# Kernel optimization log

Measured on AMD Instinct MI355X. Metric: run time of the kernel, lower is better.

The kernel has to match this reference:

```python
import jax, jax.numpy as jnp
import numpy as np

N, E, G = 50000, 800000, 2000          # nodes, edges, graphs
F_NODE, F_EDGE, H = 64, 16, 128
SLOPE = 0.01                            # leaky_relu slope used throughout AttentiveFP
NUM_ATOM_LAYERS = 2                     # num_layers=3 -> 1 GATEConv + 2 GATConv
NUM_TIMESTEPS = 3


def _leaky(v):
    return jnp.where(v >= 0, v, SLOPE * v)


def _seg_softmax(logits, seg, n):
    # PyG softmax over edges grouped by target segment
    m = jax.ops.segment_max(logits, seg, num_segments=n)
    e = jnp.exp(logits - m[seg])
    s = jax.ops.segment_sum(e, seg, num_segments=n)
    return e / (s[seg] + 1e-16)


def _gru(xi, h, Wih, Whh, bih, bhh):
    # torch.nn.GRUCell, gate order (r, z, n)
    gi = xi @ Wih.T + bih
    gh = h @ Whh.T + bhh
    ir, iz, inn = jnp.split(gi, 3, axis=-1)
    hr, hz, hn = jnp.split(gh, 3, axis=-1)
    r = jax.nn.sigmoid(ir + hr)
    z = jax.nn.sigmoid(iz + hz)
    ng = jnp.tanh(inn + r * hn)
    return (1.0 - z) * ng + z * h


def setup_inputs() -> dict:
    key = jax.random.key(0)
    ks = iter(jax.random.split(key, 64))
    def rn(shape, s=0.1):
        return jax.random.normal(next(ks), shape, jnp.float32) * s
    inp = {}
    inp["x"] = jax.random.normal(next(ks), (N, F_NODE), jnp.float32)
    inp["edge_index"] = jax.random.randint(next(ks), (2, E), 0, N)
    inp["edge_attr"] = jax.random.normal(next(ks), (E, F_EDGE), jnp.float32)
    inp["batch"] = jnp.sort(jax.random.randint(next(ks), (N,), 0, G))
    inp["lin1_W"] = rn((H, F_NODE)); inp["lin1_b"] = rn((H,))
    inp["gate_att_l"] = rn((H,)); inp["gate_att_r"] = rn((H,))
    inp["gate_lin1_W"] = rn((H, H + F_EDGE)); inp["gate_lin2_W"] = rn((H, H)); inp["gate_bias"] = rn((H,))
    inp["gru0_Wih"] = rn((3 * H, H)); inp["gru0_Whh"] = rn((3 * H, H))
    inp["gru0_bih"] = rn((3 * H,)); inp["gru0_bhh"] = rn((3 * H,))
    L = NUM_ATOM_LAYERS
    inp["atom_lin_W"] = rn((L, H, H)); inp["atom_att_src"] = rn((L, H))
    inp["atom_att_dst"] = rn((L, H)); inp["atom_bias"] = rn((L, H))
    inp["atom_gru_Wih"] = rn((L, 3 * H, H)); inp["atom_gru_Whh"] = rn((L, 3 * H, H))
    inp["atom_gru_bih"] = rn((L, 3 * H)); inp["atom_gru_bhh"] = rn((L, 3 * H))
    inp["mol_lin_W"] = rn((H, H)); inp["mol_att_src"] = rn((H,))
    inp["mol_att_dst"] = rn((H,)); inp["mol_bias"] = rn((H,))
    inp["mol_gru_Wih"] = rn((3 * H, H)); inp["mol_gru_Whh"] = rn((3 * H, H))
    inp["mol_gru_bih"] = rn((3 * H,)); inp["mol_gru_bhh"] = rn((3 * H,))
    inp["lin2_W"] = rn((H, H)); inp["lin2_b"] = rn((H,))
    inp["fin_W"] = rn((1, H)); inp["fin_b"] = rn((1,))
    return inp


def _forward(x, edge_attr, lin1_W, lin1_b, gate_att_l, gate_att_r, gate_lin1_W,
             gate_lin2_W, gate_bias, gru0_Wih, gru0_Whh, gru0_bih, gru0_bhh,
             atom_lin_W, atom_att_src, atom_att_dst, atom_bias,
             atom_gru_Wih, atom_gru_Whh, atom_gru_bih, atom_gru_bhh,
             mol_lin_W, mol_att_src, mol_att_dst, mol_bias,
             mol_gru_Wih, mol_gru_Whh, mol_gru_bih, mol_gru_bhh,
             lin2_W, lin2_b, fin_W, fin_b, edge_index, batch):
    src, dst = edge_index[0], edge_index[1]  # PyG: row=source j, col=target i
    # --- input projection ---
    x = _leaky(x @ lin1_W.T + lin1_b)                                     # [N,H]
    # --- GATEConv (edge-featured attention, add aggregation) ---
    hj = _leaky(jnp.concatenate([x[src], edge_attr], axis=-1) @ gate_lin1_W.T)  # [E,H]
    alpha = _leaky(hj @ gate_att_l + (x @ gate_att_r)[dst])               # [E]
    a = _seg_softmax(alpha, dst, N)
    h = jax.ops.segment_sum((x @ gate_lin2_W.T)[src] * a[:, None], dst, num_segments=N) + gate_bias
    h = jax.nn.elu(h)  # dropout is identity in eval mode
    x = jnp.maximum(_gru(h, x, gru0_Wih, gru0_Whh, gru0_bih, gru0_bhh), 0.0)
    # --- atom-level GATConv layers (single head, no self loops) ---
    for l in range(NUM_ATOM_LAYERS):
        xs = x @ atom_lin_W[l].T                                          # [N,H]
        a = _leaky((xs @ atom_att_src[l])[src] + (xs @ atom_att_dst[l])[dst])
        a = _seg_softmax(a, dst, N)
        h = jax.ops.segment_sum(xs[src] * a[:, None], dst, num_segments=N) + atom_bias[l]
        h = jax.nn.elu(h)
        x = jnp.maximum(_gru(h, x, atom_gru_Wih[l], atom_gru_Whh[l],
                             atom_gru_bih[l], atom_gru_bhh[l]), 0.0)
    # --- molecule-level readout: bipartite GATConv node->graph + GRU ---
    out = jnp.maximum(jax.ops.segment_sum(x, batch, num_segments=G), 0.0)  # [G,H]
    xs = x @ mol_lin_W.T                                                   # fixed sources
    a_src = xs @ mol_att_src                                               # [N]
    for _ in range(NUM_TIMESTEPS):
        od = out @ mol_lin_W.T                                             # [G,H]
        a = _leaky(a_src + (od @ mol_att_dst)[batch])
        a = _seg_softmax(a, batch, G)
        h = jax.ops.segment_sum(xs * a[:, None], batch, num_segments=G) + mol_bias
        h = jax.nn.elu(h)
        out = jnp.maximum(_gru(h, out, mol_gru_Wih, mol_gru_Whh, mol_gru_bih, mol_gru_bhh), 0.0)
    out = out @ lin2_W.T + lin2_b                                          # AttentiveFP.lin2
    return jax.nn.sigmoid(out @ fin_W.T + fin_b).squeeze(-1)               # [G]


def reference(x, edge_index, edge_attr, batch, lin1_W, lin1_b, gate_att_l, gate_att_r,
              gate_lin1_W, gate_lin2_W, gate_bias, gru0_Wih, gru0_Whh, gru0_bih, gru0_bhh,
              atom_lin_W, atom_att_src, atom_att_dst, atom_bias,
              atom_gru_Wih, atom_gru_Whh, atom_gru_bih, atom_gru_bhh,
              mol_lin_W, mol_att_src, mol_att_dst, mol_bias,
              mol_gru_Wih, mol_gru_Whh, mol_gru_bih, mol_gru_bhh,
              lin2_W, lin2_b, fin_W, fin_b):
    return _forward(x, edge_attr, lin1_W, lin1_b, gate_att_l, gate_att_r, gate_lin1_W,
                    gate_lin2_W, gate_bias, gru0_Wih, gru0_Whh, gru0_bih, gru0_bhh,
                    atom_lin_W, atom_att_src, atom_att_dst, atom_bias,
                    atom_gru_Wih, atom_gru_Whh, atom_gru_bih, atom_gru_bhh,
                    mol_lin_W, mol_att_src, mol_att_dst, mol_bias,
                    mol_gru_Wih, mol_gru_Whh, mol_gru_bih, mol_gru_bhh,
                    lin2_W, lin2_b, fin_W, fin_b, edge_index, batch)
```

## Files before the change

### kernel.cpp

```cpp
#include <hip/hip_runtime.h>
#include <math.h>

#define NN 50000
#define EE 800000
#define GG 2000
#define HH 128
#define FN 64
#define FE 16

typedef short bf16x8 __attribute__((ext_vector_type(8)));
typedef float f32x4  __attribute__((ext_vector_type(4)));

__device__ __forceinline__ float leakyf(float v){ return v>=0.f ? v : 0.01f*v; }
__device__ __forceinline__ float eluf(float v){ return v>0.f ? v : expm1f(v); }
__device__ __forceinline__ float sigmf(float v){ return 1.f/(1.f+__expf(-v)); }
__device__ __forceinline__ float tanh_fast(float x){
  float ax = fabsf(x);
  float e = __expf(-2.f*ax);
  float t = (1.f - e)/(1.f + e);
  return x>=0.f ? t : -t;
}
__device__ __forceinline__ int rdl(int v, int l){ return __builtin_amdgcn_readlane(v, l); }
__device__ __forceinline__ float rdlf(float v, int l){
  return __int_as_float(__builtin_amdgcn_readlane(__float_as_int(v), l));
}
__device__ __forceinline__ float wsum(float v){
#pragma unroll
  for(int m=32;m>=1;m>>=1) v += __shfl_xor(v,m,64);
  return v;
}
__device__ __forceinline__ float wsum16(float v){
#pragma unroll
  for(int m=8;m>=1;m>>=1) v += __shfl_xor(v,m,64);
  return v;
}
__device__ __forceinline__ float wmax64(float v){
#pragma unroll
  for(int m=32;m>=1;m>>=1) v = fmaxf(v,__shfl_xor(v,m,64));
  return v;
}

__device__ __forceinline__ f32x4 mfma16(bf16x8 a, bf16x8 b, f32x4 c){
  return __builtin_amdgcn_mfma_f32_16x16x32_bf16(a, b, c, 0, 0, 0);
}

__device__ __forceinline__ void splitbf8(const float* p, bf16x8 &hi, bf16x8 &lo){
  float4 u = *(const float4*)p;
  float4 v = *(const float4*)(p+4);
  float f[8] = {u.x,u.y,u.z,u.w,v.x,v.y,v.z,v.w};
#pragma unroll
  for(int i=0;i<8;i++){
    unsigned b = __float_as_uint(f[i]);
    unsigned ht = b & 0xFFFF0000u;
    hi[i] = (short)(b >> 16);
    float r = f[i] - __uint_as_float(ht);
    lo[i] = (short)(__float_as_uint(r) >> 16);
  }
}

#define CV_LIN1   0
#define CV_G1X    8192
#define CV_G2     24576
#define CV_ALIN   40960
#define CV_MOL    73728
#define CV_G0IH   90112
#define CV_G0HH   139264
#define CV_AIH    188416
#define CV_AHH    286720
#define CV_MIH    385024
#define CV_MHH    434176
#define CV_TOT    483328

__global__ void k_convw2(const float* __restrict__ lin1W, const float* __restrict__ glin1W,
                         const float* __restrict__ glin2W, const float* __restrict__ aLinW,
                         const float* __restrict__ aGWih, const float* __restrict__ aGWhh,
                         const float* __restrict__ mLinW, const float* __restrict__ mGWih,
                         const float* __restrict__ mGWhh, const float* __restrict__ g0Wih,
                         const float* __restrict__ g0Whh,
                         short* __restrict__ hi, short* __restrict__ lo){
  int i = blockIdx.x*256 + threadIdx.x;
  if(i >= CV_TOT) return;
  float v;
  if(i < CV_G1X){            v = lin1W[i];
  } else if(i < CV_G2){      int idx = i - CV_G1X; v = glin1W[(size_t)(idx>>7)*144 + (idx&127)];
  } else if(i < CV_ALIN){    v = glin2W[i - CV_G2];
  } else if(i < CV_MOL){     v = aLinW[i - CV_ALIN];
  } else if(i < CV_G0IH){    v = mLinW[i - CV_MOL];
  } else if(i < CV_G0HH){    v = g0Wih[i - CV_G0IH];
  } else if(i < CV_AIH){     v = g0Whh[i - CV_G0HH];
  } else if(i < CV_AHH){     v = aGWih[i - CV_AIH];
  } else if(i < CV_MIH){     v = aGWhh[i - CV_AHH];
  } else if(i < CV_MHH){     v = mGWih[i - CV_MIH];
  } else {                   v = mGWhh[i - CV_MHH];
  }
  unsigned b = __float_as_uint(v);
  unsigned ht = b & 0xFFFF0000u;
  hi[i] = (short)(b >> 16);
  float r = v - __uint_as_float(ht);
  lo[i] = (short)(__float_as_uint(r) >> 16);
}

__global__ void k_count_all(const int* __restrict__ esrc, const int* __restrict__ edst,
                            const int* __restrict__ batch,
                            int* __restrict__ degd, int* __restrict__ degs,
                            int* __restrict__ gcnt){
  int i = blockIdx.x*256 + threadIdx.x;
  if(i < EE){
    atomicAdd(&degd[edst[i]], 1);
    atomicAdd(&degs[esrc[i]], 1);
  }
  if(i < NN) atomicAdd(&gcnt[batch[i]], 1);
}

__global__ void k_scan3(const int* __restrict__ degd, const int* __restrict__ degs,
                        const int* __restrict__ gcnt,
                        int* __restrict__ eoff, int* __restrict__ soff, int* __restrict__ goff){
  __shared__ int part[1024];
  const int* cnt; int* off; int n;
  if(blockIdx.x == 0){ cnt = degd; off = eoff; n = NN; }
  else if(blockIdx.x == 1){ cnt = degs; off = soff; n = NN; }
  else { cnt = gcnt; off = goff; n = GG; }
  int t = threadIdx.x;
  int C = (n + 1023) >> 10;
  int lo = t*C, hic = min(lo + C, n);
  int s = 0;
  for(int i=lo;i<hic;i++) s += cnt[i];
  part[t] = s;
  __syncthreads();
  for(int o=1;o<1024;o<<=1){
    int v = (t>=o) ? part[t-o] : 0;
    __syncthreads();
    part[t] += v;
    __syncthreads();
  }
  int base = part[t] - s;
  int run = base;
  for(int i=lo;i<hic;i++){ run += cnt[i]; off[i+1] = run; }
  if(t==0) off[0] = 0;
}

__global__ void k_scatter2(const int* __restrict__ esrc, const int* __restrict__ edst,
                           const int* __restrict__ eoff, const int* __restrict__ soff,
                           int* __restrict__ curd, int* __restrict__ curs,
                           int* __restrict__ esrcS, int* __restrict__ eperm,
                           int* __restrict__ eord){
  int e = blockIdx.x*256 + threadIdx.x;
  if(e < EE){
    int d = edst[e];
    int pos = eoff[d] + atomicAdd(&curd[d], 1);
    esrcS[pos] = esrc[e];
    eperm[e] = pos;
    int s = esrc[e];
    int pos2 = soff[s] + atomicAdd(&curs[s], 1);
    eord[pos2] = e;
  }
}

template<int ACT, int K, int NDOT>
__global__ __launch_bounds__(256) void k_proj_mfma(const float* __restrict__ A,
                                                   const short* __restrict__ Whi,
                                                   const short* __restrict__ Wlo,
                                                   const float* __restrict__ bias,
                                                   float* __restrict__ C, int M,
                                                   const float* __restrict__ u,
                                                   const float* __restrict__ v,
                                                   float* __restrict__ douta,
                                                   float* __restrict__ doutb){
  const int wave = threadIdx.x >> 6, lane = threadIdx.x & 63;
  const int m0 = blockIdx.x*64 + wave*16;
  const int lr = lane & 15, kg = lane >> 4;
  f32x4 acc[8];
#pragma unroll
  for(int t=0;t<8;t++) acc[t] = (f32x4){0.f,0.f,0.f,0.f};

  int arow = m0 + lr;
  int ar = arow < M ? arow : (M-1);

#pragma unroll
  for(int ks=0;ks<K;ks+=32){
    const int kb = ks + kg*8;
    bf16x8 ahi, alo;
    splitbf8(&A[(size_t)ar*K + kb], ahi, alo);
#pragma unroll
    for(int t=0;t<8;t++){
      const bf16x8 bh = *(const bf16x8*)&Whi[(size_t)(t*16+lr)*K + kb];
      const bf16x8 bl = *(const bf16x8*)&Wlo[(size_t)(t*16+lr)*K + kb];
      acc[t] = mfma16(ahi, bh, acc[t]);
      acc[t] = mfma16(ahi, bl, acc[t]);
      acc[t] = mfma16(alo, bh, acc[t]);
    }
  }

  float p1[4] = {0.f,0.f,0.f,0.f};
  float p2[4] = {0.f,0.f,0.f,0.f};
#pragma unroll
  for(int t=0;t<8;t++){
    int c = t*16 + lr;
    float ut = (NDOT>=1) ? u[c] : 0.f;
    float vt = (NDOT>=2) ? v[c] : 0.f;
#pragma unroll
    for(int r=0;r<4;r++){
      int m = m0 + kg*4 + r;
      float val = acc[t][r];
      if(ACT==1) val = leakyf(val + bias[c]);
      if(m < M) C[(size_t)m*HH + c] = val;
      if(NDOT>=1) p1[r] += val*ut;
      if(NDOT>=2) p2[r] += val*vt;
    }
  }
  if(NDOT>=1){
#pragma unroll
    for(int r=0;r<4;r++){
      float s1 = wsum16(p1[r]);
      int m = m0 + kg*4 + r;
      if(lr==0 && m < M) douta[m] = s1;
      if(NDOT>=2){
        float s2 = wsum16(p2[r]);
        if(lr==0 && m < M) doutb[m] = s2;
      }
    }
  }
}

__global__ __launch_bounds__(256) void k_gru_mfma(const float* __restrict__ MSG,
                                                  const float* __restrict__ X,
                                                  const short* __restrict__ WIhi,
                                                  const short* __restrict__ WIlo,
                                                  const short* __restrict__ WHhi,
                                                  const short* __restrict__ WHlo,
                                                  const float* __restrict__ bih,
                                                  const float* __restrict__ bhh,
                                                  float* __restrict__ XOUT, int M){
  __shared__ short LW[12*16*128];
  const int tid = threadIdx.x;
  const int wave = tid >> 6, lane = tid & 63;
  const int m0 = blockIdx.x*64 + wave*16;
  const int lr = lane & 15, kg = lane >> 4;
  int arow = m0 + lr;
  int ar = arow < M ? arow : (M-1);

  bf16x8 mh[4], ml[4], xh[4], xl[4];
#pragma unroll
  for(int ks=0;ks<4;ks++){
    splitbf8(&MSG[(size_t)ar*HH + ks*32 + kg*8], mh[ks], ml[ks]);
    splitbf8(&X  [(size_t)ar*HH + ks*32 + kg*8], xh[ks], xl[ks]);
  }

  const int srow = tid >> 4;
  const int scb  = tid & 15;
  const int sdst = srow*128 + ((scb ^ (srow & 7))*8);
  const size_t sgoff = (size_t)srow*HH + scb*8;

#pragma unroll 1
  for(int t=0;t<8;t++){
#pragma unroll
    for(int r=0;r<12;r++){
      const short* mat = (r<3) ? WIhi : (r<6) ? WHhi : (r<9) ? WIlo : WHlo;
      const int g = (r % 3);
      const short* src = mat + (size_t)(g*128 + t*16)*HH + sgoff;
      *(bf16x8*)&LW[r*2048 + sdst] = *(const bf16x8*)src;
    }
    __syncthreads();

    f32x4 aIr = (f32x4){0.f,0.f,0.f,0.f}, aIz = aIr, aIn = aIr;
    f32x4 aHr = aIr, aHz = aIr, aHn = aIr;
#pragma unroll
    for(int ks=0;ks<4;ks++){
      const int cb = ks*4 + kg;
      const int rb = lr*128 + ((cb ^ (lr & 7))*8);
      bf16x8 bIrh = *(const bf16x8*)&LW[ 0*2048 + rb];
      bf16x8 bIzh = *(const bf16x8*)&LW[ 1*2048 + rb];
      bf16x8 bInh = *(const bf16x8*)&LW[ 2*2048 + rb];
      bf16x8 bHrh = *(const bf16x8*)&LW[ 3*2048 + rb];
      bf16x8 bHzh = *(const bf16x8*)&LW[ 4*2048 + rb];
      bf16x8 bHnh = *(const bf16x8*)&LW[ 5*2048 + rb];
      bf16x8 bIrl = *(const bf16x8*)&LW[ 6*2048 + rb];
      bf16x8 bIzl = *(const bf16x8*)&LW[ 7*2048 + rb];
      bf16x8 bInl = *(const bf16x8*)&LW[ 8*2048 + rb];
      bf16x8 bHrl = *(const bf16x8*)&LW[ 9*2048 + rb];
      bf16x8 bHzl = *(const bf16x8*)&LW[10*2048 + rb];
      bf16x8 bHnl = *(const bf16x8*)&LW[11*2048 + rb];
      aIr = mfma16(mh[ks], bIrh, aIr); aIr = mfma16(mh[ks], bIrl, aIr); aIr = mfma16(ml[ks], bIrh, aIr);
      aIz = mfma16(mh[ks], bIzh, aIz); aIz = mfma16(mh[ks], bIzl, aIz); aIz = mfma16(ml[ks], bIzh, aIz);
      aIn = mfma16(mh[ks], bInh, aIn); aIn = mfma16(mh[ks], bInl, aIn); aIn = mfma16(ml[ks], bInh, aIn);
      aHr = mfma16(xh[ks], bHrh, aHr); aHr = mfma16(xh[ks], bHrl, aHr); aHr = mfma16(xl[ks], bHrh, aHr);
      aHz = mfma16(xh[ks], bHzh, aHz); aHz = mfma16(xh[ks], bHzl, aHz); aHz = mfma16(xl[ks], bHzh, aHz);
      aHn = mfma16(xh[ks], bHnh, aHn); aHn = mfma16(xh[ks], bHnl, aHn); aHn = mfma16(xl[ks], bHnh, aHn);
    }

    const int c = t*16 + lr;
    const float bir = bih[c], biz = bih[c+HH], bin = bih[c+2*HH];
    const float bhr = bhh[c], bhz = bhh[c+HH], bhn = bhh[c+2*HH];
#pragma unroll
    for(int r=0;r<4;r++){
      int mm = m0 + kg*4 + r;
      if(mm < M){
        float ir = aIr[r]+bir, iz = aIz[r]+biz, in_ = aIn[r]+bin;
        float hr = aHr[r]+bhr, hz = aHz[r]+bhz, hn = aHn[r]+bhn;
        float rr = sigmf(ir + hr);
        float z  = sigmf(iz + hz);
        float ng = tanh_fast(in_ + rr*hn);
        float hp = X[(size_t)mm*HH + c];
        XOUT[(size_t)mm*HH + c] = fmaxf((1.f - z)*ng + z*hp, 0.f);
      }
    }
    __syncthreads();
  }
}

__global__ __launch_bounds__(256) void k_gate_alpha3(const float* __restrict__ XP,
                                                     const float* __restrict__ EA,
                                                     const int* __restrict__ esrc,
                                                     const int* __restrict__ edst,
                                                     const float* __restrict__ W1,
                                                     const float* __restrict__ attl,
                                                     const float* __restrict__ RD,
                                                     const int* __restrict__ eperm,
                                                     const int* __restrict__ eord,
                                                     float* __restrict__ ALPHA){
  __shared__ float W1E[128*16];
  __shared__ float ATTL[128];
  const int tid = threadIdx.x;
#pragma unroll
  for(int q=0;q<8;q++){
    int idx = tid*8 + q;
    int c = idx >> 4, f = idx & 15;
    W1E[idx] = W1[(size_t)c*144 + 128 + f];
  }
  if(tid < 128) ATTL[tid] = attl[tid];
  __syncthreads();

  const int p = blockIdx.x*256 + tid;
  const int eo = eord[p];
  const int s  = esrc[eo];
  const int d  = edst[eo];
  const int pd = eperm[eo];

  float ea[16];
  {
    const float4* g = (const float4*)&EA[(size_t)eo*FE];
    float4 v0=g[0], v1=g[1], v2=g[2], v3=g[3];
    ea[0]=v0.x;ea[1]=v0.y;ea[2]=v0.z;ea[3]=v0.w;
    ea[4]=v1.x;ea[5]=v1.y;ea[6]=v1.z;ea[7]=v1.w;
    ea[8]=v2.x;ea[9]=v2.y;ea[10]=v2.z;ea[11]=v2.w;
    ea[12]=v3.x;ea[13]=v3.y;ea[14]=v3.z;ea[15]=v3.w;
  }

  float acc = 0.f;
#pragma unroll 4
  for(int c0=0;c0<HH;c0+=4){
    float4 xp = *(const float4*)&XP[(size_t)s*HH + c0];
    float xpv[4] = {xp.x, xp.y, xp.z, xp.w};
#pragma unroll
    for(int cc=0;cc<4;cc++){
      const float* wr = &W1E[(c0+cc)*16];
      float eaw = 0.f;
#pragma unroll
      for(int f=0;f<16;f++) eaw += ea[f]*wr[f];
      acc += leakyf(xpv[cc] + eaw) * ATTL[c0+cc];
    }
  }
  ALPHA[pd] = leakyf(acc + RD[d]);
}

template<int MODE>
__global__ void k_softmaxw(const int* __restrict__ off, const int* __restrict__ items,
                           const float* __restrict__ AIN, const float* __restrict__ A1,
                           const float* __restrict__ A2, float* __restrict__ WOUT, int nseg){
  int w = (blockIdx.x*blockDim.x + threadIdx.x) >> 6;
  int lane = threadIdx.x & 63;
  if(w >= nseg) return;
  int s0 = off[w], s1 = off[w+1];
  int n = s1 - s0;
  float a2 = (MODE==0) ? 0.f : A2[w];

  if(n <= 64){
    float a = -INFINITY;
    int i = s0 + lane;
    if(lane < n){
      if(MODE==0) a = AIN[i];
      else if(MODE==1) a = leakyf(A1[items[i]] + a2);
      else a = leakyf(A1[i] + a2);
    }
    float m = wmax64(a);
    float e = (lane < n) ? __expf(a - m) : 0.f;
    float s = wsum(e);
    if(lane < n) WOUT[i] = e/(s + 1e-16f);
    return;
  }

  float m = -INFINITY;
  for(int i=s0+lane;i<s1;i+=64){
    float a;
    if(MODE==0) a = AIN[i];
    else if(MODE==1) a = leakyf(A1[items[i]] + a2);
    else a = leakyf(A1[i] + a2);
    m = fmaxf(m, a);
  }
  m = wmax64(m);

  float s = 0.f;
  for(int i=s0+lane;i<s1;i+=64){
    float a;
    if(MODE==0) a = AIN[i];
    else if(MODE==1) a = leakyf(A1[items[i]] + a2);
    else a = leakyf(A1[i] + a2);
    s += __expf(a - m);
  }
  s = wsum(s);
  float inv = 1.f/(s + 1e-16f);

  for(int i=s0+lane;i<s1;i+=64){
    float a;
    if(MODE==0) a = AIN[i];
    else if(MODE==1) a = leakyf(A1[items[i]] + a2);
    else a = leakyf(A1[i] + a2);
    WOUT[i] = __expf(a - m)*inv;
  }
}

__global__ void k_gather(const int* __restrict__ off, const int* __restrict__ items,
                         const float* __restrict__ W, const float* __restrict__ XSrc,
                         const float* __restrict__ bias, float* __restrict__ OUT, int nseg){
  int w = (blockIdx.x*blockDim.x + threadIdx.x) >> 6;
  int lane = threadIdx.x & 63;
  if(w >= nseg) return;
  int s0 = off[w], s1 = off[w+1];
  float hx = 0.f, hy = 0.f;

  for(int c0=s0;c0<s1;c0+=64){
    int n = min(64, s1-c0);
    int it = 0; float wg = 0.f;
    if(lane < n){
      int i = c0 + lane;
      it = items ? items[i] : i;
      wg = W[i];
    }
#pragma unroll 16
    for(int j=0;j<n;j++){
      int itj = rdl(it, j);
      float wj = rdlf(wg, j);
      float2 xv = *(const float2*)&XSrc[(size_t)itj*HH + 2*lane];
      hx += wj*xv.x;
      hy += wj*xv.y;
    }
  }
  float2 bv = *(const float2*)&bias[2*lane];
  float2 o;
  o.x = eluf(hx + bv.x);
  o.y = eluf(hy + bv.y);
  *(float2*)&OUT[(size_t)w*HH + 2*lane] = o;
}

__global__ void k_dot2(const float* __restrict__ X, const float* __restrict__ u,
                       float* __restrict__ a, int M){
  int w = (blockIdx.x*blockDim.x + threadIdx.x) >> 6;
  int lane = threadIdx.x & 63;
  if(w >= M) return;
  float2 x = *(const float2*)&X[(size_t)w*HH + 2*lane];
  float2 uu = *(const float2*)&u[2*lane];
  float p = x.x*uu.x + x.y*uu.y;
  p = wsum(p);
  if(lane==0) a[w] = p;
}

__global__ void k_ginit(const int* __restrict__ goff, const float* __restrict__ X,
                        float* __restrict__ OUT){
  int g = (blockIdx.x*blockDim.x + threadIdx.x) >> 6;
  int lane = threadIdx.x & 63;
  if(g >= GG) return;
  int s0 = goff[g], s1 = goff[g+1];
  float hx=0.f, hy=0.f;
  for(int n=s0;n<s1;n++){
    float2 xv = *(const float2*)&X[(size_t)n*HH + 2*lane];
    hx += xv.x; hy += xv.y;
  }
  float2 o;
  o.x = fmaxf(hx, 0.f);
  o.y = fmaxf(hy, 0.f);
  *(float2*)&OUT[(size_t)g*HH + 2*lane] = o;
}

__global__ void k_weff(const float* __restrict__ lin2W, const float* __restrict__ lin2b,
                       const float* __restrict__ finW, const float* __restrict__ finb,
                       const float* __restrict__ mLinW, const float* __restrict__ mAttD,
                       float* __restrict__ weff){
  int c = threadIdx.x;
  float s = 0.f, q = 0.f;
  for(int j=0;j<HH;j++){
    s += finW[j]*lin2W[(size_t)j*HH + c];
    q += mAttD[j]*mLinW[(size_t)j*HH + c];
  }
  weff[c] = s;
  weff[256 + c] = q;
  if(c==0){
    float bb = finb[0];
    for(int j=0;j<HH;j++) bb += lin2b[j]*finW[j];
    weff[HH] = bb;
  }
}

__global__ void k_final(const float* __restrict__ OUT, const float* __restrict__ weff,
                        float* __restrict__ y){
  int g = (blockIdx.x*blockDim.x + threadIdx.x) >> 6;
  int lane = threadIdx.x & 63;
  if(g >= GG) return;
  float2 ov = *(const float2*)&OUT[(size_t)g*HH + 2*lane];
  float2 wv = *(const float2*)&weff[2*lane];
  float p = ov.x*wv.x + ov.y*wv.y;
  p = wsum(p);
  if(lane==0) y[g] = sigmf(p + weff[HH]);
}

extern "C" void kernel_launch(void* const* d_in, const int* in_sizes, int n_in,
                              void* d_out, int out_size, void* d_ws, size_t ws_size,
                              hipStream_t stream){
  const float* in_x   = (const float*)d_in[0];
  const int*   eidx   = (const int*)d_in[1];
  const float* ea     = (const float*)d_in[2];
  const int*   batch  = (const int*)d_in[3];
  const float* lin1W  = (const float*)d_in[4];
  const float* lin1b  = (const float*)d_in[5];
  const float* gattl  = (const float*)d_in[6];
  const float* gattr  = (const float*)d_in[7];
  const float* glin1W = (const float*)d_in[8];
  const float* glin2W = (const float*)d_in[9];
  const float* gbias  = (const float*)d_in[10];
  const float* g0Wih  = (const float*)d_in[11];
  const float* g0Whh  = (const float*)d_in[12];
  const float* g0bih  = (const float*)d_in[13];
  const float* g0bhh  = (const float*)d_in[14];
  const float* aLinW  = (const float*)d_in[15];
  const float* aAttS  = (const float*)d_in[16];
  const float* aAttD  = (const float*)d_in[17];
  const float* aBias  = (const float*)d_in[18];
  const float* aGWih  = (const float*)d_in[19];
  const float* aGWhh  = (const float*)d_in[20];
  const float* aGbih  = (const float*)d_in[21];
  const float* aGbhh  = (const float*)d_in[22];
  const float* mLinW  = (const float*)d_in[23];
  const float* mAttS  = (const float*)d_in[24];
  const float* mAttD  = (const float*)d_in[25];
  const float* mBias  = (const float*)d_in[26];
  const float* mGWih  = (const float*)d_in[27];
  const float* mGWhh  = (const float*)d_in[28];
  const float* mGbih  = (const float*)d_in[29];
  const float* mGbhh  = (const float*)d_in[30];
  const float* lin2W  = (const float*)d_in[31];
  const float* lin2b  = (const float*)d_in[32];
  const float* finW   = (const float*)d_in[33];
  const float* finb   = (const float*)d_in[34];

  const int* esrc0 = eidx;
  const int* edst0 = eidx + EE;

  char* w = (char*)d_ws;
  size_t o = 0;
  auto alloc = [&](size_t bytes)->void*{
    void* p = w + o;
    o = (o + bytes + 255) & ~(size_t)255;
    return p;
  };
  float* X    = (float*)alloc((size_t)NN*HH*4);
  float* XB   = (float*)alloc((size_t)NN*HH*4);
  float* XS   = (float*)alloc((size_t)NN*HH*4);
  float* MSG  = (float*)alloc((size_t)NN*HH*4);
  float* XP   = (float*)alloc((size_t)NN*HH*4);
  float* ALPHA= (float*)alloc((size_t)EE*4);
  float* S1   = (float*)alloc((size_t)NN*4);
  float* S2   = (float*)alloc((size_t)NN*4);
  float* ADSTG= (float*)alloc((size_t)GG*4);
  float* OUTg = (float*)alloc((size_t)GG*HH*4);
  float* OUTb = (float*)alloc((size_t)GG*HH*4);
  float* HG   = (float*)alloc((size_t)GG*HH*4);
  float* WEFF = (float*)alloc(512*4);
  short* cWhi = (short*)alloc((size_t)CV_TOT*2);
  short* cWlo = (short*)alloc((size_t)CV_TOT*2);
  int* zeroreg= (int*)alloc((size_t)(4*NN + 2048)*4);
  int* degd = zeroreg;
  int* degs = zeroreg + NN;
  int* curd = zeroreg + 2*NN;
  int* curs = zeroreg + 3*NN;
  int* gcnt = zeroreg + 4*NN;
  int* eoff = (int*)alloc((size_t)(NN+1)*4);
  int* soff = (int*)alloc((size_t)(NN+1)*4);
  int* goff = (int*)alloc((size_t)(GG+1)*4);
  int* esrcS= (int*)alloc((size_t)EE*4);
  int* eperm= (int*)alloc((size_t)EE*4);
  int* eord = (int*)alloc((size_t)EE*4);

  const short* c_lin1_h = cWhi + CV_LIN1; const short* c_lin1_l = cWlo + CV_LIN1;
  const short* c_g1x_h  = cWhi + CV_G1X;  const short* c_g1x_l  = cWlo + CV_G1X;
  const short* c_g2_h   = cWhi + CV_G2;   const short* c_g2_l   = cWlo + CV_G2;
  const short* c_mol_h  = cWhi + CV_MOL;  const short* c_mol_l  = cWlo + CV_MOL;
  const short* c_g0ih_h = cWhi + CV_G0IH; const short* c_g0ih_l = cWlo + CV_G0IH;
  const short* c_g0hh_h = cWhi + CV_G0HH; const short* c_g0hh_l = cWlo + CV_G0HH;
  const short* c_mih_h  = cWhi + CV_MIH;  const short* c_mih_l  = cWlo + CV_MIH;
  const short* c_mhh_h  = cWhi + CV_MHH;  const short* c_mhh_l  = cWlo + CV_MHH;

  k_convw2<<<(CV_TOT+255)/256, 256, 0, stream>>>(lin1W, glin1W, glin2W, aLinW, aGWih, aGWhh,
                                                 mLinW, mGWih, mGWhh, g0Wih, g0Whh, cWhi, cWlo);
  k_weff<<<1, 128, 0, stream>>>(lin2W, lin2b, finW, finb, mLinW, mAttD, WEFF);

  hipMemsetAsync(zeroreg, 0, (size_t)(4*NN + 2048)*4, stream);
  k_count_all<<<EE/256, 256, 0, stream>>>(esrc0, edst0, batch, degd, degs, gcnt);
  k_scan3<<<3, 1024, 0, stream>>>(degd, degs, gcnt, eoff, soff, goff);
  k_scatter2<<<EE/256, 256, 0, stream>>>(esrc0, edst0, eoff, soff, curd, curs, esrcS, eperm, eord);

  const int gN = (NN + 63)/64;
  const int gG = (GG + 63)/64;

  k_proj_mfma<1,64,1><<<gN, 256, 0, stream>>>(in_x, c_lin1_h, c_lin1_l, lin1b, X, NN,
                                              gattr, nullptr, S1, nullptr);

  k_proj_mfma<0,128,0><<<gN, 256, 0, stream>>>(X, c_g1x_h, c_g1x_l, nullptr, XP, NN,
                                               nullptr, nullptr, nullptr, nullptr);
  k_proj_mfma<0,128,0><<<gN, 256, 0, stream>>>(X, c_g2_h, c_g2_l, nullptr, XS, NN,
                                               nullptr, nullptr, nullptr, nullptr);
  k_gate_alpha3<<<EE/256, 256, 0, stream>>>(XP, ea, esrc0, edst0, glin1W, gattl, S1,
                                            eperm, eord, ALPHA);
  k_softmaxw<0><<<(NN+3)/4, 256, 0, stream>>>(eoff, nullptr, ALPHA, nullptr, nullptr, ALPHA, NN);
  k_gather<<<(NN+3)/4, 256, 0, stream>>>(eoff, esrcS, ALPHA, XS, gbias, MSG, NN);
  k_gru_mfma<<<gN, 256, 0, stream>>>(MSG, X, c_g0ih_h, c_g0ih_l, c_g0hh_h, c_g0hh_l,
                                     g0bih, g0bhh, XB, NN);
  { float* t = X; X = XB; XB = t; }

  for(int l=0;l<2;l++){
    const short* c_a_h   = cWhi + CV_ALIN + (size_t)l*HH*HH;
    const short* c_a_l   = cWlo + CV_ALIN + (size_t)l*HH*HH;
    const short* c_aih_h = cWhi + CV_AIH + (size_t)l*3*HH*HH;
    const short* c_aih_l = cWlo + CV_AIH + (size_t)l*3*HH*HH;
    const short* c_ahh_h = cWhi + CV_AHH + (size_t)l*3*HH*HH;
    const short* c_ahh_l = cWlo + CV_AHH + (size_t)l*3*HH*HH;
    const float* asl  = aAttS + (size_t)l*HH;
    const float* adl  = aAttD + (size_t)l*HH;
    const float* bl   = aBias + (size_t)l*HH;
    const float* bi   = aGbih + (size_t)l*3*HH;
    const float* bh   = aGbhh + (size_t)l*3*HH;
    k_proj_mfma<0,128,2><<<gN, 256, 0, stream>>>(X, c_a_h, c_a_l, nullptr, XS, NN,
                                                 asl, adl, S1, S2);
    k_softmaxw<1><<<(NN+3)/4, 256, 0, stream>>>(eoff, esrcS, nullptr, S1, S2, ALPHA, NN);
    k_gather<<<(NN+3)/4, 256, 0, stream>>>(eoff, esrcS, ALPHA, XS, bl, MSG, NN);
    k_gru_mfma<<<gN, 256, 0, stream>>>(MSG, X, c_aih_h, c_aih_l, c_ahh_h, c_ahh_l, bi, bh, XB, NN);
    { float* t = X; X = XB; XB = t; }
  }

  k_ginit<<<(GG+3)/4, 256, 0, stream>>>(goff, X, OUTg);
  k_proj_mfma<0,128,1><<<gN, 256, 0, stream>>>(X, c_mol_h, c_mol_l, nullptr, XS, NN,
                                               mAttS, nullptr, S1, nullptr);

  float* Ocur = OUTg;
  float* Onxt = OUTb;
  for(int t=0;t<3;t++){
    k_dot2<<<(GG+3)/4, 256, 0, stream>>>(Ocur, WEFF+256, ADSTG, GG);
    k_softmaxw<2><<<(GG+3)/4, 256, 0, stream>>>(goff, nullptr, nullptr, S1, ADSTG, ALPHA, GG);
    k_gather<<<(GG+3)/4, 256, 0, stream>>>(goff, nullptr, ALPHA, XS, mBias, HG, GG);
    k_gru_mfma<<<gG, 256, 0, stream>>>(HG, Ocur, c_mih_h, c_mih_l, c_mhh_h, c_mhh_l,
                                       mGbih, mGbhh, Onxt, GG);
    { float* tt = Ocur; Ocur = Onxt; Onxt = tt; }
  }

  k_final<<<(GG+3)/4, 256, 0, stream>>>(Ocur, WEFF, (float*)d_out);
}
```

Before: 1.296 ms.

## Compute gate edge-attribute projection with split-bf16 MFMA in gate alpha kernel

The per-edge 16x128 edge-attribute projection in the GATE attention-logit kernel moves from scalar FMAs against a shared-memory weight tile to MFMA 16x16 instructions. It uses a hi/lo bf16 split (three-term product) to keep near-fp32 accuracy, and the weight is pre-split in the conversion kernel. Each wavefront now handles 16-edge tiles, reads XP per column with lane-strided coalesced loads, and reduces partial logits with a 16-lane sum. This removes the 2048 scalar FMAs per edge, at the cost of more index reloads and a loop over 8 tiles per wave.

```diff
diff --git a/kernel.cpp b/kernel.cpp
--- a/kernel.cpp
+++ b/kernel.cpp
@@ -69,7 +69,8 @@
 #define CV_AHH    286720
 #define CV_MIH    385024
 #define CV_MHH    434176
-#define CV_TOT    483328
+#define CV_GE     483328
+#define CV_TOT2   485376
 
 __global__ void k_convw2(const float* __restrict__ lin1W, const float* __restrict__ glin1W,
                          const float* __restrict__ glin2W, const float* __restrict__ aLinW,
@@ -79,7 +80,7 @@
                          const float* __restrict__ g0Whh,
                          short* __restrict__ hi, short* __restrict__ lo){
   int i = blockIdx.x*256 + threadIdx.x;
-  if(i >= CV_TOT) return;
+  if(i >= CV_TOT2) return;
   float v;
   if(i < CV_G1X){            v = lin1W[i];
   } else if(i < CV_G2){      int idx = i - CV_G1X; v = glin1W[(size_t)(idx>>7)*144 + (idx&127)];
@@ -91,7 +92,8 @@
   } else if(i < CV_AHH){     v = aGWih[i - CV_AIH];
   } else if(i < CV_MIH){     v = aGWhh[i - CV_AHH];
   } else if(i < CV_MHH){     v = mGWih[i - CV_MIH];
-  } else {                   v = mGWhh[i - CV_MHH];
+  } else if(i < CV_GE){      v = mGWhh[i - CV_MHH];
+  } else {                   int idx = i - CV_GE; v = glin1W[(size_t)(idx>>4)*144 + 128 + (idx&15)];
   }
   unsigned b = __float_as_uint(v);
   unsigned ht = b & 0xFFFF0000u;
@@ -308,59 +310,71 @@
   }
 }
 
-__global__ __launch_bounds__(256) void k_gate_alpha3(const float* __restrict__ XP,
+__global__ __launch_bounds__(256) void k_gate_alpha4(const float* __restrict__ XP,
                                                      const float* __restrict__ EA,
                                                      const int* __restrict__ esrc,
                                                      const int* __restrict__ edst,
-                                                     const float* __restrict__ W1,
+                                                     const short* __restrict__ GEhi,
+                                                     const short* __restrict__ GElo,
                                                      const float* __restrict__ attl,
                                                      const float* __restrict__ RD,
                                                      const int* __restrict__ eperm,
                                                      const int* __restrict__ eord,
                                                      float* __restrict__ ALPHA){
-  __shared__ float W1E[128*16];
-  __shared__ float ATTL[128];
-  const int tid = threadIdx.x;
-#pragma unroll
-  for(int q=0;q<8;q++){
-    int idx = tid*8 + q;
-    int c = idx >> 4, f = idx & 15;
-    W1E[idx] = W1[(size_t)c*144 + 128 + f];
-  }
-  if(tid < 128) ATTL[tid] = attl[tid];
-  __syncthreads();
-
-  const int p = blockIdx.x*256 + tid;
-  const int eo = eord[p];
-  const int s  = esrc[eo];
-  const int d  = edst[eo];
-  const int pd = eperm[eo];
-
-  float ea[16];
-  {
-    const float4* g = (const float4*)&EA[(size_t)eo*FE];
-    float4 v0=g[0], v1=g[1], v2=g[2], v3=g[3];
-    ea[0]=v0.x;ea[1]=v0.y;ea[2]=v0.z;ea[3]=v0.w;
-    ea[4]=v1.x;ea[5]=v1.y;ea[6]=v1.z;ea[7]=v1.w;
-    ea[8]=v2.x;ea[9]=v2.y;ea[10]=v2.z;ea[11]=v2.w;
-    ea[12]=v3.x;ea[13]=v3.y;ea[14]=v3.z;ea[15]=v3.w;
-  }
-
-  float acc = 0.f;
-#pragma unroll 4
-  for(int c0=0;c0<HH;c0+=4){
-    float4 xp = *(const float4*)&XP[(size_t)s*HH + c0];
-    float xpv[4] = {xp.x, xp.y, xp.z, xp.w};
-#pragma unroll
-    for(int cc=0;cc<4;cc++){
-      const float* wr = &W1E[(c0+cc)*16];
-      float eaw = 0.f;
-#pragma unroll
-      for(int f=0;f<16;f++) eaw += ea[f]*wr[f];
-      acc += leakyf(xpv[cc] + eaw) * ATTL[c0+cc];
-    }
-  }
-  ALPHA[pd] = leakyf(acc + RD[d]);
+  const int lane = threadIdx.x & 63;
+  const int wid = (blockIdx.x*256 + threadIdx.x) >> 6;
+  if(wid >= EE/128) return;
+  const int lr = lane & 15, kg = lane >> 4;
+
+  bf16x8 B1[8], B2[8];
+#pragma unroll
+  for(int t=0;t<8;t++){
+    const int col = t*16 + lr;
+    B1[t] = *(const bf16x8*)&GEhi[col*16 + (kg&1)*8];
+    B2[t] = *(const bf16x8*)&GElo[col*16 + (kg&1)*8];
+  }
+  float at[8];
+#pragma unroll
+  for(int t=0;t<8;t++) at[t] = attl[t*16 + lr];
+
+#pragma unroll 1
+  for(int tw = wid*8; tw < wid*8 + 8; ++tw){
+    const int p0 = tw*16;
+    const int eoA = eord[p0 + lr];
+    bf16x8 hi8, lo8;
+    splitbf8(&EA[(size_t)eoA*FE + (kg&1)*8], hi8, lo8);
+    bf16x8 A1 = (kg < 2) ? hi8 : lo8;
+    bf16x8 A2 = hi8;
+    if(kg >= 2){
+#pragma unroll
+      for(int i=0;i<8;i++) A2[i] = 0;
+    }
+    int srcR[4];
+#pragma unroll
+    for(int r=0;r<4;r++) srcR[r] = esrc[eord[p0 + kg*4 + r]];
+
+    float p[4] = {0.f,0.f,0.f,0.f};
+#pragma unroll
+    for(int t=0;t<8;t++){
+      f32x4 acc = (f32x4){0.f,0.f,0.f,0.f};
+      acc = mfma16(A2, B2[t], acc);
+      acc = mfma16(A1, B1[t], acc);
+      const int c = t*16 + lr;
+#pragma unroll
+      for(int r=0;r<4;r++){
+        float xp = XP[(size_t)srcR[r]*HH + c];
+        p[r] += leakyf(acc[r] + xp) * at[t];
+      }
+    }
+#pragma unroll
+    for(int r=0;r<4;r++){
+      float s = wsum16(p[r]);
+      if(lr == 0){
+        const int eoj = eord[p0 + kg*4 + r];
+        ALPHA[eperm[eoj]] = leakyf(s + RD[edst[eoj]]);
+      }
+    }
+  }
 }
 
 template<int MODE>
@@ -574,8 +588,8 @@
   float* OUTb = (float*)alloc((size_t)GG*HH*4);
   float* HG   = (float*)alloc((size_t)GG*HH*4);
   float* WEFF = (float*)alloc(512*4);
-  short* cWhi = (short*)alloc((size_t)CV_TOT*2);
-  short* cWlo = (short*)alloc((size_t)CV_TOT*2);
+  short* cWhi = (short*)alloc((size_t)CV_TOT2*2);
+  short* cWlo = (short*)alloc((size_t)CV_TOT2*2);
   int* zeroreg= (int*)alloc((size_t)(4*NN + 2048)*4);
   int* degd = zeroreg;
   int* degs = zeroreg + NN;
@@ -597,9 +611,10 @@
   const short* c_g0hh_h = cWhi + CV_G0HH; const short* c_g0hh_l = cWlo + CV_G0HH;
   const short* c_mih_h  = cWhi + CV_MIH;  const short* c_mih_l  = cWlo + CV_MIH;
   const short* c_mhh_h  = cWhi + CV_MHH;  const short* c_mhh_l  = cWlo + CV_MHH;
-
-  k_convw2<<<(CV_TOT+255)/256, 256, 0, stream>>>(lin1W, glin1W, glin2W, aLinW, aGWih, aGWhh,
-                                                 mLinW, mGWih, mGWhh, g0Wih, g0Whh, cWhi, cWlo);
+  const short* c_ge_h   = cWhi + CV_GE;   const short* c_ge_l   = cWlo + CV_GE;
+
+  k_convw2<<<(CV_TOT2+255)/256, 256, 0, stream>>>(lin1W, glin1W, glin2W, aLinW, aGWih, aGWhh,
+                                                  mLinW, mGWih, mGWhh, g0Wih, g0Whh, cWhi, cWlo);
   k_weff<<<1, 128, 0, stream>>>(lin2W, lin2b, finW, finb, mLinW, mAttD, WEFF);
 
   hipMemsetAsync(zeroreg, 0, (size_t)(4*NN + 2048)*4, stream);
@@ -617,8 +632,8 @@
                                                nullptr, nullptr, nullptr, nullptr);
   k_proj_mfma<0,128,0><<<gN, 256, 0, stream>>>(X, c_g2_h, c_g2_l, nullptr, XS, NN,
                                                nullptr, nullptr, nullptr, nullptr);
-  k_gate_alpha3<<<EE/256, 256, 0, stream>>>(XP, ea, esrc0, edst0, glin1W, gattl, S1,
-                                            eperm, eord, ALPHA);
+  k_gate_alpha4<<<(EE/128 + 3)/4, 256, 0, stream>>>(XP, ea, esrc0, edst0, c_ge_h, c_ge_l,
+                                                    gattl, S1, eperm, eord, ALPHA);
   k_softmaxw<0><<<(NN+3)/4, 256, 0, stream>>>(eoff, nullptr, ALPHA, nullptr, nullptr, ALPHA, NN);
   k_gather<<<(NN+3)/4, 256, 0, stream>>>(eoff, esrcS, ALPHA, XS, gbias, MSG, NN);
   k_gru_mfma<<<gN, 256, 0, stream>>>(MSG, X, c_g0ih_h, c_g0ih_l, c_g0hh_h, c_g0hh_l,
```

New measurement: 1.351 ms. 4.3% more time.
